# Kernel tuning notes

Hardware: AMD Instinct MI355X
Metric: run time of the kernel (lower is better)

## Reference

```python
import jax, jax.numpy as jnp
import numpy as np

B, CIN, H, W = 2, 192, 56, 56
ODIM, HEADS, K, PAD, STRIDE = 192, 6, 7, 3, 1


def setup_inputs() -> dict:
    key = jax.random.key(0)
    ks = jax.random.split(key, 6)
    w_scale = 0.02
    return {
        "x": jax.random.normal(ks[0], (B, CIN, H, W), dtype=jnp.float32),
        "wq": jax.random.normal(ks[1], (ODIM, CIN), dtype=jnp.float32) * w_scale,
        "wk": jax.random.normal(ks[2], (ODIM, CIN), dtype=jnp.float32) * w_scale,
        "wv": jax.random.normal(ks[3], (ODIM, CIN), dtype=jnp.float32) * w_scale,
        "pos_embedding": jax.random.normal(ks[4], (1, 2 * K - 1), dtype=jnp.float32),
        "w_proj": jax.random.normal(ks[5], (ODIM, ODIM), dtype=jnp.float32) * w_scale,
        "kernel_size": K,
        "padding": PAD,
        "stride": STRIDE,
        "num_heads": HEADS,
    }


def _patches(x, k, pad, stride):
    # torch.nn.Unfold(kernel_size=k, padding=pad, stride=stride), kept as
    # (B, C, k*k, oh, ow) with window offsets ordered row-major (i*k + j),
    # channel slowest -- matching torch's (C, kh, kw) flattening.
    xp = jnp.pad(x, ((0, 0), (0, 0), (pad, pad), (pad, pad)))
    Hp, Wp = xp.shape[2], xp.shape[3]
    oh = (Hp - k) // stride + 1
    ow = (Wp - k) // stride + 1
    sl = [xp[:, :, i:i + stride * (oh - 1) + 1:stride, j:j + stride * (ow - 1) + 1:stride]
          for i in range(k) for j in range(k)]
    return jnp.stack(sl, axis=2)


def reference(x, wq, wk, wv, pos_embedding, w_proj, kernel_size, padding, stride, num_heads):
    b, c, h, w = x.shape
    # 1x1 convs (no bias) == channel matmuls
    q = jnp.einsum('oc,bchw->bohw', wq, x)
    k = jnp.einsum('oc,bchw->bohw', wk, x)
    v = jnp.einsum('oc,bchw->bohw', wv, x)
    # Unfold(kernel=1, stride=s) on q == strided spatial subsampling
    q = q[:, :, ::stride, ::stride]
    kp = _patches(k, kernel_size, padding, stride)  # (B, O, K*K, oh, ow)
    vp = _patches(v, kernel_size, padding, stride)
    oh, ow = kp.shape[3], kp.shape[4]
    d = wq.shape[0] // num_heads
    kk = kernel_size * kernel_size
    qh = q.reshape(b, num_heads, d, oh, ow)
    kh = kp.reshape(b, num_heads, d, kk, oh, ow)
    vh = vp.reshape(b, num_heads, d, kk, oh, ow)
    # per-pixel windowed attention scores: (B, heads, K*K, oh, ow)
    attn = jnp.einsum('bhdij,bhdkij->bhkij', qh, kh)
    # relative position bias: index = row_offset + col_offset (0 .. 2K-2)
    coords = np.arange(kernel_size)
    rel = (coords[:, None] + coords[None, :]).reshape(-1)  # (K*K,)
    bias = pos_embedding[0][jnp.asarray(rel)]  # (K*K,)
    attn = jax.nn.softmax(attn + bias[None, None, :, None, None], axis=2)
    out = jnp.einsum('bhkij,bhdkij->bhdij', attn, vh)
    out = out.reshape(b, num_heads * d, oh, ow)
    return jnp.einsum('oc,bchw->bohw', w_proj, out)
```

## Files before the change

### kernel.cpp

```cpp
#include <hip/hip_runtime.h>


#define HW    3136
#define WIMG  56
#define CIN   192
#define QKVLD 576
#define SMEM_P1 53312
#define SMEM_P2 43904
#define LOG2E 1.44269504088896340736f

using short8 = __attribute__((ext_vector_type(8))) short;
using f32x4  = __attribute__((ext_vector_type(4))) float;

__device__ __forceinline__ unsigned pack2(float a, float b) {
    unsigned r;
    asm("v_cvt_pk_bf16_f32 %0, %1, %2" : "=v"(r) : "v"(a), "v"(b));
    return r;
}
__device__ __forceinline__ float bflo(unsigned u) {
    union { unsigned u; float f; } v; v.u = u << 16; return v.f;
}
__device__ __forceinline__ float bfhi(unsigned u) {
    union { unsigned u; float f; } v; v.u = u & 0xffff0000u; return v.f;
}
__device__ __forceinline__ float dot2bf(unsigned k2, unsigned q2, float c) {
    float d;
    asm("v_dot2_f32_bf16 %0, %1, %2, %3" : "=v"(d) : "v"(k2), "v"(q2), "v"(c));
    return d;
}
__device__ __forceinline__ float2 pkfma(float2 a, float2 b, float2 c) {
    float2 d;
    asm("v_pk_fma_f32 %0, %1, %2, %3" : "=v"(d) : "v"(a), "v"(b), "v"(c));
    return d;
}
__device__ __forceinline__ float qsum4(float s) {
    union { float f; int i; } u, t;
    u.f = s;
    t.i = __builtin_amdgcn_update_dpp(0, u.i, 0xB1, 0xF, 0xF, true);
    u.f += t.f;
    t.i = __builtin_amdgcn_update_dpp(0, u.i, 0x4E, 0xF, 0xF, true);
    u.f += t.f;
    return u.f;
}

__global__ __launch_bounds__(256) void k_p1(
    const float* __restrict__ x, const float* __restrict__ wq,
    const float* __restrict__ wk, const float* __restrict__ wv,
    unsigned short* __restrict__ qkv)
{
    extern __shared__ char smem[];
    unsigned short* As  = (unsigned short*)smem;
    unsigned short* Bs  = As + 64 * 200;
    unsigned*       Asw = (unsigned*)smem;
    unsigned*       Bsw = (unsigned*)(smem + 25600);

    const int tid = threadIdx.x;
    const int lane = tid & 63, wave = tid >> 6;
    const int l15  = lane & 15, quad = lane >> 4;
    const int wm   = (wave & 1) * 32, wn = (wave >> 1) * 32;

    const int t = blockIdx.x;
    const int mt = t % 98, nt = t / 98;
    const int m0 = mt * 64, n0 = nt * 64;
    const float* Wp = (nt < 3) ? (wq + (size_t)n0 * CIN)
                    : (nt < 6) ? (wk + (size_t)(n0 - 192) * CIN)
                               : (wv + (size_t)(n0 - 384) * CIN);

    #pragma unroll
    for (int i = 0; i < 6; ++i) {
        int u = tid + 256 * i;
        int pq = u & 15, c2 = u >> 4;
        int pp = m0 + pq * 4;
        int bb = (pp >= HW) ? 1 : 0;
        const float* src = x + ((size_t)(bb * CIN + c2 * 2)) * HW + (pp - bb * HW);
        float4 f0 = *(const float4*)src;
        float4 f1 = *(const float4*)(src + HW);
        Asw[(pq * 4 + 0) * 100 + c2] = pack2(f0.x, f1.x);
        Asw[(pq * 4 + 1) * 100 + c2] = pack2(f0.y, f1.y);
        Asw[(pq * 4 + 2) * 100 + c2] = pack2(f0.z, f1.z);
        Asw[(pq * 4 + 3) * 100 + c2] = pack2(f0.w, f1.w);
    }
    {
        int o = tid >> 2, c4 = tid & 3;
        #pragma unroll
        for (int i = 0; i < 12; ++i) {
            int cq = c4 + 4 * i;
            float4 w = *(const float4*)(Wp + (size_t)o * CIN + cq * 4);
            uint2 d; d.x = pack2(w.x, w.y); d.y = pack2(w.z, w.w);
            *(uint2*)(Bsw + o * 100 + cq * 2) = d;
        }
    }
    __syncthreads();

    f32x4 acc[2][2] = {};
    const unsigned short* pa0 = As + (wm + l15) * 200 + quad * 8;
    const unsigned short* pb0 = Bs + (wn + l15) * 200 + quad * 8;
    #pragma unroll
    for (int s = 0; s < 6; ++s) {
        short8 a0 = *(const short8*)(pa0 + s * 32);
        short8 a1 = *(const short8*)(pa0 + 16 * 200 + s * 32);
        short8 b0 = *(const short8*)(pb0 + s * 32);
        short8 b1 = *(const short8*)(pb0 + 16 * 200 + s * 32);
        acc[0][0] = __builtin_amdgcn_mfma_f32_16x16x32_bf16(a0, b0, acc[0][0], 0, 0, 0);
        acc[0][1] = __builtin_amdgcn_mfma_f32_16x16x32_bf16(a0, b1, acc[0][1], 0, 0, 0);
        acc[1][0] = __builtin_amdgcn_mfma_f32_16x16x32_bf16(a1, b0, acc[1][0], 0, 0, 0);
        acc[1][1] = __builtin_amdgcn_mfma_f32_16x16x32_bf16(a1, b1, acc[1][1], 0, 0, 0);
    }

    const int gm = m0 + wm + quad * 4;
    const int gn = n0 + wn + l15;
    #pragma unroll
    for (int ti = 0; ti < 2; ++ti)
        #pragma unroll
        for (int tj = 0; tj < 2; ++tj)
            #pragma unroll
            for (int rr = 0; rr < 4; rr += 2) {
                unsigned r = pack2(acc[ti][tj][rr], acc[ti][tj][rr + 1]);
                qkv[(size_t)(gm + ti * 16 + rr) * QKVLD + (gn + tj * 16)] =
                    (unsigned short)r;
                qkv[(size_t)(gm + ti * 16 + rr + 1) * QKVLD + (gn + tj * 16)] =
                    (unsigned short)(r >> 16);
            }
}

__global__ __launch_bounds__(256) void k_p2(
    const unsigned short* __restrict__ qkv, const float* __restrict__ pos,
    unsigned short* __restrict__ oact)
{
    extern __shared__ char smem[];
    unsigned short* kbufB = (unsigned short*)smem;
    float*          vbuf  = (float*)(smem + 196 * 40 * 2);

    const int tid = threadIdx.x;
    const int t = blockIdx.x;
    const int tz = t / 49, r49 = t - tz * 49;
    const int ty = r49 / 7, tx = r49 - ty * 7;
    const int bq = tz / 6, h = tz - bq * 6;
    const int y0 = ty * 8 - 3, x0 = tx * 8 - 3;

    const int sub = tid & 3, pix = tid >> 2;
    const int py = pix >> 3, px = pix & 7;
    const int y = ty * 8 + py, xx = tx * 8 + px;
    const int p = y * WIMG + xx;

    uint4 qv = *(const uint4*)(qkv + (size_t)(bq * HW + p) * QKVLD + h * 32 + sub * 8);
    float posE[13];
    #pragma unroll
    for (int i = 0; i < 13; ++i) posE[i] = pos[i] * LOG2E;

    #pragma unroll
    for (int i = 0; i < 7; ++i) {
        int u = tid + 256 * i;
        if (u < 1568) {
            int pp = u >> 3, uu = u & 7;
            int part = uu >> 2, sub8 = uu & 3;
            int ppy = pp / 14, ppx = pp - ppy * 14;
            int gy = y0 + ppy, gx = x0 + ppx;
            uint4 rv = make_uint4(0u, 0u, 0u, 0u);
            if ((unsigned)gy < 56u && (unsigned)gx < 56u)
                rv = *(const uint4*)(qkv +
                    (size_t)(bq * HW + gy * WIMG + gx) * QKVLD +
                    192 + part * 192 + h * 32 + sub8 * 8);
            if (part == 0) {
                *(uint4*)(kbufB + pp * 40 + sub8 * 8) = rv;
            } else {
                float4 vA, vB;
                vA.x=bflo(rv.x); vA.y=bfhi(rv.x); vA.z=bflo(rv.y); vA.w=bfhi(rv.y);
                vB.x=bflo(rv.z); vB.y=bfhi(rv.z); vB.z=bflo(rv.w); vB.w=bfhi(rv.w);
                float* dst = vbuf + pp * 36 + sub8 * 8;
                *(float4*)(dst + 0) = vA;
                *(float4*)(dst + 4) = vB;
            }
        }
    }
    __syncthreads();

    const unsigned short* kr = kbufB + sub * 8;

    float logits[49];
    #pragma unroll
    for (int kk = 0; kk < 49; ++kk) {
        const int ky = kk / 7, kx = kk % 7;
        const int pp = (py + ky) * 14 + (px + kx);
        uint4 kv = *(const uint4*)(kr + pp * 40);
        float s = 0.f;
        s = dot2bf(kv.x, qv.x, s);
        s = dot2bf(kv.y, qv.y, s);
        s = dot2bf(kv.z, qv.z, s);
        s = dot2bf(kv.w, qv.w, s);
        logits[kk] = fmaf(qsum4(s), LOG2E, posE[ky + kx]);
    }

    float m = logits[0];
    #pragma unroll
    for (int kk = 1; kk < 49; ++kk) m = fmaxf(m, logits[kk]);
    float sum = 0.f;
    #pragma unroll
    for (int kk = 0; kk < 49; ++kk) {
        logits[kk] = __builtin_amdgcn_exp2f(logits[kk] - m);
        sum += logits[kk];
    }

    float2 a01 = make_float2(0.f, 0.f), a23 = make_float2(0.f, 0.f);
    float2 a45 = make_float2(0.f, 0.f), a67 = make_float2(0.f, 0.f);
    #pragma unroll
    for (int kk = 0; kk < 49; ++kk) {
        const int ky = kk / 7, kx = kk % 7;
        const int pp = (py + ky) * 14 + (px + kx);
        const float4* vp = (const float4*)(vbuf + pp * 36 + sub * 8);
        float4 vA = vp[0], vB = vp[1];
        const float pw = logits[kk];
        const float2 pw2 = make_float2(pw, pw);
        a01 = pkfma(make_float2(vA.x, vA.y), pw2, a01);
        a23 = pkfma(make_float2(vA.z, vA.w), pw2, a23);
        a45 = pkfma(make_float2(vB.x, vB.y), pw2, a45);
        a67 = pkfma(make_float2(vB.z, vB.w), pw2, a67);
    }
    const float inv = 1.f / sum;

    uint4 o;
    o.x = pack2(a01.x * inv, a01.y * inv);
    o.y = pack2(a23.x * inv, a23.y * inv);
    o.z = pack2(a45.x * inv, a45.y * inv);
    o.w = pack2(a67.x * inv, a67.y * inv);
    *(uint4*)(oact + (size_t)(bq * HW + p) * CIN + h * 32 + sub * 8) = o;
}

__global__ __launch_bounds__(256) void k_p3(
    const float* __restrict__ wproj, const unsigned short* __restrict__ oact,
    float* __restrict__ out)
{
    extern __shared__ char smem[];
    unsigned short* As  = (unsigned short*)smem;
    unsigned short* Bs  = As + 64 * 200;
    unsigned*       Asw = (unsigned*)smem;

    const int tid = threadIdx.x;
    const int lane = tid & 63, wave = tid >> 6;
    const int l15  = lane & 15, quad = lane >> 4;
    const int wm   = (wave & 1) * 32, wn = (wave >> 1) * 32;

    const int t = blockIdx.x;
    const int mt = t % 3, pt = t / 3;
    {
        int o = tid >> 2, c4 = tid & 3;
        #pragma unroll
        for (int i = 0; i < 12; ++i) {
            int cq = c4 + 4 * i;
            float4 w = *(const float4*)(wproj + (size_t)(mt * 64 + o) * CIN + cq * 4);
            uint2 d; d.x = pack2(w.x, w.y); d.y = pack2(w.z, w.w);
            *(uint2*)(Asw + o * 100 + cq * 2) = d;
        }
    }
    {
        int rw = tid >> 2, s4 = tid & 3;
        #pragma unroll
        for (int i = 0; i < 6; ++i) {
            int seg = s4 + 4 * i;
            uint4 dv = *(const uint4*)(oact + (size_t)(pt * 64 + rw) * CIN + seg * 8);
            *(uint4*)(Bs + rw * 200 + seg * 8) = dv;
        }
    }
    __syncthreads();

    f32x4 acc[2][2] = {};
    const unsigned short* pa0 = As + (wm + l15) * 200 + quad * 8;
    const unsigned short* pb0 = Bs + (wn + l15) * 200 + quad * 8;
    #pragma unroll
    for (int s = 0; s < 6; ++s) {
        short8 a0 = *(const short8*)(pa0 + s * 32);
        short8 a1 = *(const short8*)(pa0 + 16 * 200 + s * 32);
        short8 b0 = *(const short8*)(pb0 + s * 32);
        short8 b1 = *(const short8*)(pb0 + 16 * 200 + s * 32);
        acc[0][0] = __builtin_amdgcn_mfma_f32_16x16x32_bf16(a0, b0, acc[0][0], 0, 0, 0);
        acc[0][1] = __builtin_amdgcn_mfma_f32_16x16x32_bf16(a0, b1, acc[0][1], 0, 0, 0);
        acc[1][0] = __builtin_amdgcn_mfma_f32_16x16x32_bf16(a1, b0, acc[1][0], 0, 0, 0);
        acc[1][1] = __builtin_amdgcn_mfma_f32_16x16x32_bf16(a1, b1, acc[1][1], 0, 0, 0);
    }

    const int bb = (pt * 64 >= HW) ? 1 : 0;
    const int pl = pt * 64 - bb * HW + wn + l15;
    const int go = mt * 64 + wm + quad * 4;
    float* Yb = out + (size_t)bb * (CIN * HW);
    #pragma unroll
    for (int ti = 0; ti < 2; ++ti)
        #pragma unroll
        for (int tj = 0; tj < 2; ++tj)
            #pragma unroll
            for (int rr = 0; rr < 4; ++rr)
                Yb[(size_t)(go + ti * 16 + rr) * HW + pl + tj * 16] = acc[ti][tj][rr];
}

extern "C" void kernel_launch(void* const* d_in, const int* in_sizes, int n_in,
                              void* d_out, int out_size, void* d_ws, size_t ws_size,
                              hipStream_t stream)
{
    const float* x     = (const float*)d_in[0];
    const float* wq    = (const float*)d_in[1];
    const float* wk    = (const float*)d_in[2];
    const float* wv    = (const float*)d_in[3];
    const float* pos   = (const float*)d_in[4];
    const float* wproj = (const float*)d_in[5];

    char* ws = (char*)d_ws;
    unsigned short* qkvp  = (unsigned short*)ws;
    unsigned short* oactp = (unsigned short*)(ws + 7225344);
    float*          outp  = (float*)d_out;

    k_p1<<<dim3(882), dim3(256), SMEM_P1, stream>>>(x, wq, wk, wv, qkvp);
    k_p2<<<dim3(588), dim3(256), SMEM_P2, stream>>>(qkvp, pos, oactp);
    k_p3<<<dim3(294), dim3(256), SMEM_P1, stream>>>(wproj, oactp, outp);
}
```

Baseline: 104.0 us.

## Store V as fp16 column pairs and use dot2 for attention-weighted sum

The attention kernel now stores V in shared memory as fp16 values that interleave adjacent column pairs, where it previously held fp32. The weighted sum uses v_dot2_f32_f16 on pairs of window columns, with weights packed per row and parity-dependent zero padding. This halves V shared-memory footprint and LDS reads and reduces FMA count. The cost is that the probabilities and V pass through fp16 with round-toward-zero conversion. The QKV GEMM's A tile stride is also padded from 200 to 202 to reduce LDS bank conflicts.

```diff
diff --git a/kernel.cpp b/kernel.cpp
--- a/kernel.cpp
+++ b/kernel.cpp
@@ -5,8 +5,8 @@
 #define WIMG  56
 #define CIN   192
 #define QKVLD 576
-#define SMEM_P1 53312
-#define SMEM_P2 43904
+#define SMEM_P1 51456
+#define SMEM_P2 29792
 #define LOG2E 1.44269504088896340736f
 
 using short8 = __attribute__((ext_vector_type(8))) short;
@@ -17,6 +17,11 @@
     asm("v_cvt_pk_bf16_f32 %0, %1, %2" : "=v"(r) : "v"(a), "v"(b));
     return r;
 }
+__device__ __forceinline__ unsigned pkh(float a, float b) {
+    unsigned r;
+    asm("v_cvt_pkrtz_f16_f32 %0, %1, %2" : "=v"(r) : "v"(a), "v"(b));
+    return r;
+}
 __device__ __forceinline__ float bflo(unsigned u) {
     union { unsigned u; float f; } v; v.u = u << 16; return v.f;
 }
@@ -28,9 +33,9 @@
     asm("v_dot2_f32_bf16 %0, %1, %2, %3" : "=v"(d) : "v"(k2), "v"(q2), "v"(c));
     return d;
 }
-__device__ __forceinline__ float2 pkfma(float2 a, float2 b, float2 c) {
-    float2 d;
-    asm("v_pk_fma_f32 %0, %1, %2, %3" : "=v"(d) : "v"(a), "v"(b), "v"(c));
+__device__ __forceinline__ float dot2h(unsigned v2, unsigned w2, float c) {
+    float d;
+    asm("v_dot2_f32_f16 %0, %1, %2, %3" : "=v"(d) : "v"(v2), "v"(w2), "v"(c));
     return d;
 }
 __device__ __forceinline__ float qsum4(float s) {
@@ -50,9 +55,9 @@
 {
     extern __shared__ char smem[];
     unsigned short* As  = (unsigned short*)smem;
-    unsigned short* Bs  = As + 64 * 200;
+    unsigned short* Bs  = As + 64 * 202;
     unsigned*       Asw = (unsigned*)smem;
-    unsigned*       Bsw = (unsigned*)(smem + 25600);
+    unsigned*       Bsw = (unsigned*)(smem + 25856);
 
     const int tid = threadIdx.x;
     const int lane = tid & 63, wave = tid >> 6;
@@ -75,10 +80,10 @@
         const float* src = x + ((size_t)(bb * CIN + c2 * 2)) * HW + (pp - bb * HW);
         float4 f0 = *(const float4*)src;
         float4 f1 = *(const float4*)(src + HW);
-        Asw[(pq * 4 + 0) * 100 + c2] = pack2(f0.x, f1.x);
-        Asw[(pq * 4 + 1) * 100 + c2] = pack2(f0.y, f1.y);
-        Asw[(pq * 4 + 2) * 100 + c2] = pack2(f0.z, f1.z);
-        Asw[(pq * 4 + 3) * 100 + c2] = pack2(f0.w, f1.w);
+        Asw[(pq * 4 + 0) * 101 + c2] = pack2(f0.x, f1.x);
+        Asw[(pq * 4 + 1) * 101 + c2] = pack2(f0.y, f1.y);
+        Asw[(pq * 4 + 2) * 101 + c2] = pack2(f0.z, f1.z);
+        Asw[(pq * 4 + 3) * 101 + c2] = pack2(f0.w, f1.w);
     }
     {
         int o = tid >> 2, c4 = tid & 3;
@@ -93,12 +98,12 @@
     __syncthreads();
 
     f32x4 acc[2][2] = {};
-    const unsigned short* pa0 = As + (wm + l15) * 200 + quad * 8;
+    const unsigned short* pa0 = As + (wm + l15) * 202 + quad * 8;
     const unsigned short* pb0 = Bs + (wn + l15) * 200 + quad * 8;
     #pragma unroll
     for (int s = 0; s < 6; ++s) {
         short8 a0 = *(const short8*)(pa0 + s * 32);
-        short8 a1 = *(const short8*)(pa0 + 16 * 200 + s * 32);
+        short8 a1 = *(const short8*)(pa0 + 16 * 202 + s * 32);
         short8 b0 = *(const short8*)(pb0 + s * 32);
         short8 b1 = *(const short8*)(pb0 + 16 * 200 + s * 32);
         acc[0][0] = __builtin_amdgcn_mfma_f32_16x16x32_bf16(a0, b0, acc[0][0], 0, 0, 0);
@@ -129,7 +134,7 @@
 {
     extern __shared__ char smem[];
     unsigned short* kbufB = (unsigned short*)smem;
-    float*          vbuf  = (float*)(smem + 196 * 40 * 2);
+    unsigned*       vpb   = (unsigned*)(smem + 196 * 40 * 2);
 
     const int tid = threadIdx.x;
     const int t = blockIdx.x;
@@ -149,28 +154,40 @@
     for (int i = 0; i < 13; ++i) posE[i] = pos[i] * LOG2E;
 
     #pragma unroll
-    for (int i = 0; i < 7; ++i) {
+    for (int i = 0; i < 5; ++i) {
         int u = tid + 256 * i;
-        if (u < 1568) {
-            int pp = u >> 3, uu = u & 7;
-            int part = uu >> 2, sub8 = uu & 3;
+        if (u < 784) {
+            int pp = u >> 2, sub8 = u & 3;
             int ppy = pp / 14, ppx = pp - ppy * 14;
             int gy = y0 + ppy, gx = x0 + ppx;
             uint4 rv = make_uint4(0u, 0u, 0u, 0u);
             if ((unsigned)gy < 56u && (unsigned)gx < 56u)
                 rv = *(const uint4*)(qkv +
                     (size_t)(bq * HW + gy * WIMG + gx) * QKVLD +
-                    192 + part * 192 + h * 32 + sub8 * 8);
-            if (part == 0) {
-                *(uint4*)(kbufB + pp * 40 + sub8 * 8) = rv;
-            } else {
-                float4 vA, vB;
-                vA.x=bflo(rv.x); vA.y=bfhi(rv.x); vA.z=bflo(rv.y); vA.w=bfhi(rv.y);
-                vB.x=bflo(rv.z); vB.y=bfhi(rv.z); vB.z=bflo(rv.w); vB.w=bfhi(rv.w);
-                float* dst = vbuf + pp * 36 + sub8 * 8;
-                *(float4*)(dst + 0) = vA;
-                *(float4*)(dst + 4) = vB;
-            }
+                    192 + h * 32 + sub8 * 8);
+            *(uint4*)(kbufB + pp * 40 + sub8 * 8) = rv;
+        } else if (u < 1176) {
+            int vu = u - 784;
+            int pr = vu >> 2, cg = vu & 3;
+            int rowy = pr / 7, pc = pr - rowy * 7;
+            int gy = y0 + rowy, gxe = x0 + 2 * pc;
+            uint4 a = make_uint4(0u,0u,0u,0u), b = make_uint4(0u,0u,0u,0u);
+            const bool oky = (unsigned)gy < 56u;
+            const unsigned short* vs = qkv +
+                (size_t)(bq * HW + gy * WIMG + gxe) * QKVLD + 384 + h * 32 + cg * 8;
+            if (oky && (unsigned)gxe < 56u)       a = *(const uint4*)vs;
+            if (oky && (unsigned)(gxe + 1) < 56u) b = *(const uint4*)(vs + QKVLD);
+            unsigned d0 = pkh(bflo(a.x), bflo(b.x));
+            unsigned d1 = pkh(bfhi(a.x), bfhi(b.x));
+            unsigned d2 = pkh(bflo(a.y), bflo(b.y));
+            unsigned d3 = pkh(bfhi(a.y), bfhi(b.y));
+            unsigned d4 = pkh(bflo(a.z), bflo(b.z));
+            unsigned d5 = pkh(bfhi(a.z), bfhi(b.z));
+            unsigned d6 = pkh(bflo(a.w), bflo(b.w));
+            unsigned d7 = pkh(bfhi(a.w), bfhi(b.w));
+            unsigned* dst = vpb + pr * 36 + cg * 8;
+            *(uint4*)(dst)     = make_uint4(d0, d1, d2, d3);
+            *(uint4*)(dst + 4) = make_uint4(d4, d5, d6, d7);
         }
     }
     __syncthreads();
@@ -201,28 +218,59 @@
         sum += logits[kk];
     }
 
-    float2 a01 = make_float2(0.f, 0.f), a23 = make_float2(0.f, 0.f);
-    float2 a45 = make_float2(0.f, 0.f), a67 = make_float2(0.f, 0.f);
-    #pragma unroll
-    for (int kk = 0; kk < 49; ++kk) {
-        const int ky = kk / 7, kx = kk % 7;
-        const int pp = (py + ky) * 14 + (px + kx);
-        const float4* vp = (const float4*)(vbuf + pp * 36 + sub * 8);
-        float4 vA = vp[0], vB = vp[1];
-        const float pw = logits[kk];
-        const float2 pw2 = make_float2(pw, pw);
-        a01 = pkfma(make_float2(vA.x, vA.y), pw2, a01);
-        a23 = pkfma(make_float2(vA.z, vA.w), pw2, a23);
-        a45 = pkfma(make_float2(vB.x, vB.y), pw2, a45);
-        a67 = pkfma(make_float2(vB.z, vB.w), pw2, a67);
+    const int e = px & 1, pb = px >> 1;
+    const unsigned* vr = vpb + sub * 8;
+    float a0=0,a1=0,a2=0,a3=0,a4=0,a5=0,a6=0,a7=0;
+    #pragma unroll
+    for (int ky = 0; ky < 7; ++ky) {
+        const float* w = logits + ky * 7;
+        float l0 = e ? 0.f  : w[0], h0 = e ? w[0] : w[1];
+        float l1 = e ? w[1] : w[2], h1 = e ? w[2] : w[3];
+        float l2 = e ? w[3] : w[4], h2 = e ? w[4] : w[5];
+        float l3 = e ? w[5] : w[6], h3 = e ? w[6] : 0.f;
+        unsigned wd0 = pkh(l0, h0), wd1 = pkh(l1, h1);
+        unsigned wd2 = pkh(l2, h2), wd3 = pkh(l3, h3);
+        const unsigned* vb = vr + ((py + ky) * 7 + pb) * 36;
+        {
+            const uint4* q4 = (const uint4*)vb;
+            uint4 A = q4[0], B4 = q4[1];
+            a0=dot2h(A.x,wd0,a0);  a1=dot2h(A.y,wd0,a1);
+            a2=dot2h(A.z,wd0,a2);  a3=dot2h(A.w,wd0,a3);
+            a4=dot2h(B4.x,wd0,a4); a5=dot2h(B4.y,wd0,a5);
+            a6=dot2h(B4.z,wd0,a6); a7=dot2h(B4.w,wd0,a7);
+        }
+        {
+            const uint4* q4 = (const uint4*)(vb + 36);
+            uint4 A = q4[0], B4 = q4[1];
+            a0=dot2h(A.x,wd1,a0);  a1=dot2h(A.y,wd1,a1);
+            a2=dot2h(A.z,wd1,a2);  a3=dot2h(A.w,wd1,a3);
+            a4=dot2h(B4.x,wd1,a4); a5=dot2h(B4.y,wd1,a5);
+            a6=dot2h(B4.z,wd1,a6); a7=dot2h(B4.w,wd1,a7);
+        }
+        {
+            const uint4* q4 = (const uint4*)(vb + 72);
+            uint4 A = q4[0], B4 = q4[1];
+            a0=dot2h(A.x,wd2,a0);  a1=dot2h(A.y,wd2,a1);
+            a2=dot2h(A.z,wd2,a2);  a3=dot2h(A.w,wd2,a3);
+            a4=dot2h(B4.x,wd2,a4); a5=dot2h(B4.y,wd2,a5);
+            a6=dot2h(B4.z,wd2,a6); a7=dot2h(B4.w,wd2,a7);
+        }
+        {
+            const uint4* q4 = (const uint4*)(vb + 108);
+            uint4 A = q4[0], B4 = q4[1];
+            a0=dot2h(A.x,wd3,a0);  a1=dot2h(A.y,wd3,a1);
+            a2=dot2h(A.z,wd3,a2);  a3=dot2h(A.w,wd3,a3);
+            a4=dot2h(B4.x,wd3,a4); a5=dot2h(B4.y,wd3,a5);
+            a6=dot2h(B4.z,wd3,a6); a7=dot2h(B4.w,wd3,a7);
+        }
     }
     const float inv = 1.f / sum;
 
     uint4 o;
-    o.x = pack2(a01.x * inv, a01.y * inv);
-    o.y = pack2(a23.x * inv, a23.y * inv);
-    o.z = pack2(a45.x * inv, a45.y * inv);
-    o.w = pack2(a67.x * inv, a67.y * inv);
+    o.x = pack2(a0 * inv, a1 * inv);
+    o.y = pack2(a2 * inv, a3 * inv);
+    o.z = pack2(a4 * inv, a5 * inv);
+    o.w = pack2(a6 * inv, a7 * inv);
     *(uint4*)(oact + (size_t)(bq * HW + p) * CIN + h * 32 + sub * 8) = o;
 }
 
```

Result: slower. 106.6 us (+2.5%).
